# Performance work log

Hardware: AMD Instinct MI355X
Metric: run time of the kernel (lower is better)

## Reference

```python
import jax, jax.numpy as jnp
import numpy as np

B, T, R = 64, 256, 256          # batch, timepoints, n_rois (T==R required by bmm path)
H, NH, DH, FF, LAT, L = 256, 8, 32, 512, 64, 2
EPS = 1e-5


def layernorm(x, g, b):
    m = x.mean(-1, keepdims=True)
    v = ((x - m) ** 2).mean(-1, keepdims=True)
    return (x - m) / jnp.sqrt(v + EPS) * g + b


def leaky_relu(x):
    return jnp.where(x >= 0, x, 0.1 * x)


def setup_inputs() -> dict:
    key = jax.random.key(0)
    ks = iter(jax.random.split(key, 64))
    def nrm(shape, s=0.02):
        return jax.random.normal(next(ks), shape, jnp.float32) * s
    return {
        "x": jax.random.normal(next(ks), (B, T, R), jnp.float32),
        "node_view": jax.random.normal(next(ks), (B, R, R), jnp.float32) * 0.1,
        "edge_view": jax.random.normal(next(ks), (B, R, R), jnp.float32) * 0.1,
        "fp_w": nrm((H, R)), "fp_b": jnp.zeros((H,)),
        "fp_g": jnp.ones((H,)), "fp_beta": jnp.zeros((H,)),
        "qkv_w": nrm((L, 3 * H, H)), "qkv_b": jnp.zeros((L, 3 * H)),
        "attn_out_w": nrm((L, H, H)), "attn_out_b": jnp.zeros((L, H)),
        "ln1_g": jnp.ones((L, H)), "ln1_b": jnp.zeros((L, H)),
        "ff1_w": nrm((L, FF, H)), "ff1_b": jnp.zeros((L, FF)),
        "ff2_w": nrm((L, H, FF)), "ff2_b": jnp.zeros((L, H)),
        "ln2_g": jnp.ones((L, H)), "ln2_b": jnp.zeros((L, H)),
        "out_w": nrm((R, H)), "out_b": jnp.zeros((R,)),
        "mu_w1": nrm((H // 2, H)), "mu_b1": jnp.zeros((H // 2,)),
        "mu_g": jnp.ones((H // 2,)), "mu_beta": jnp.zeros((H // 2,)),
        "mu_w2": nrm((LAT, H // 2)), "mu_b2": jnp.zeros((LAT,)),
        "lv_w1": nrm((H // 2, H)), "lv_b1": jnp.zeros((H // 2,)),
        "lv_g": jnp.ones((H // 2,)), "lv_beta": jnp.zeros((H // 2,)),
        "lv_w2": nrm((LAT, H // 2)), "lv_b2": jnp.zeros((LAT,)),
    }


def reference(x, node_view, edge_view, fp_w, fp_b, fp_g, fp_beta,
              qkv_w, qkv_b, attn_out_w, attn_out_b, ln1_g, ln1_b,
              ff1_w, ff1_b, ff2_w, ff2_b, ln2_g, ln2_b,
              out_w, out_b, mu_w1, mu_b1, mu_g, mu_beta, mu_w2, mu_b2,
              lv_w1, lv_b1, lv_g, lv_beta, lv_w2, lv_b2):
    # graph-view message passing: bmm(x^T, view), averaged, transposed back
    xr = jnp.swapaxes(x, 1, 2)                           # [B,R,T]
    msg = 0.5 * (jnp.einsum('brt,btq->brq', xr, node_view)
                 + jnp.einsum('brt,btq->brq', xr, edge_view))
    h = jnp.swapaxes(msg, 1, 2)                          # [B,T,R]
    # feature_proj: Linear -> LayerNorm -> LeakyReLU(0.1) -> Dropout(eval)
    h = leaky_relu(layernorm(h @ fp_w.T + fp_b, fp_g, fp_beta))  # [B,T,H]
    # TransformerEncoder (post-norm, relu FFN, dropout=identity)
    scale = 1.0 / jnp.sqrt(jnp.float32(DH))
    for i in range(L):
        qkv = h @ qkv_w[i].T + qkv_b[i]                  # [B,T,3H]
        q, k, v = jnp.split(qkv, 3, axis=-1)
        q = q.reshape(B, T, NH, DH).transpose(0, 2, 1, 3)
        k = k.reshape(B, T, NH, DH).transpose(0, 2, 1, 3)
        v = v.reshape(B, T, NH, DH).transpose(0, 2, 1, 3)
        attn = jax.nn.softmax(jnp.einsum('bhqd,bhkd->bhqk', q, k) * scale, axis=-1)
        o = jnp.einsum('bhqk,bhkd->bhqd', attn, v).transpose(0, 2, 1, 3).reshape(B, T, H)
        o = o @ attn_out_w[i].T + attn_out_b[i]
        h = layernorm(h + o, ln1_g[i], ln1_b[i])
        f = jax.nn.relu(h @ ff1_w[i].T + ff1_b[i]) @ ff2_w[i].T + ff2_b[i]
        h = layernorm(h + f, ln2_g[i], ln2_b[i])
    # fresh linear (treated as fixed params) then batched Pearson correlation
    y = h @ out_w.T + out_b                              # [B,T,R]
    data = jnp.swapaxes(y, 1, 2)                         # [B,R,T]
    c = data - data.mean(-1, keepdims=True)
    std = jnp.sqrt((c ** 2).sum(-1, keepdims=True) / (T - 1))   # unbiased, like torch.std
    cn = c / (std + 1e-8)
    corr = jnp.einsum('brt,bst->brs', cn, cn) / (T - 1)
    corr = jnp.nan_to_num(jnp.clip(corr, -1.0, 1.0), nan=0.0)   # [B,R,R]
    # heads
    pooled = h.mean(axis=1)                              # [B,H]
    mu = leaky_relu(layernorm(pooled @ mu_w1.T + mu_b1, mu_g, mu_beta)) @ mu_w2.T + mu_b2
    logvar = leaky_relu(layernorm(pooled @ lv_w1.T + lv_b1, lv_g, lv_beta)) @ lv_w2.T + lv_b2
    return mu, logvar, corr
```

## Files before the change

kernel.cpp:

```cpp
#include <hip/hip_runtime.h>
#include <hip/hip_bf16.h>
#include <math.h>

#define BB 64
#define NLAYER 2

typedef __attribute__((ext_vector_type(8))) short bfrag;
typedef __attribute__((ext_vector_type(4))) float f4_t;

__device__ __forceinline__ float dot4(float4 a, float4 b, float acc) {
    acc = fmaf(a.x, b.x, acc);
    acc = fmaf(a.y, b.y, acc);
    acc = fmaf(a.z, b.z, acc);
    acc = fmaf(a.w, b.w, acc);
    return acc;
}

__device__ __forceinline__ ushort f2bf(float f) {
    uint32_t u = __float_as_uint(f);
    uint32_t r = (u + 0x7FFFu + ((u >> 16) & 1u)) >> 16;
    return (ushort)r;
}
__device__ __forceinline__ float bf2f(ushort u) {
    return __uint_as_float(((uint32_t)u) << 16);
}

__global__ __launch_bounds__(256) void k_cvt(
    const float* __restrict__ fp_w, const float* __restrict__ qkv_w,
    const float* __restrict__ aow, const float* __restrict__ f1w,
    const float* __restrict__ f2w, const float* __restrict__ outw,
    ushort* __restrict__ dst) {
    const int g = blockIdx.x;
    const size_t idx = (size_t)g * 2048 + threadIdx.x * 8;
    const float* src;
    size_t base;
    if (g < 32)       { src = fp_w;  base = 0; }
    else if (g < 224) { src = qkv_w; base = 65536; }
    else if (g < 288) { src = aow;   base = 458752; }
    else if (g < 416) { src = f1w;   base = 589824; }
    else if (g < 544) { src = f2w;   base = 851968; }
    else              { src = outw;  base = 1114112; }
    const float4* s4 = reinterpret_cast<const float4*>(src + (idx - base));
    float4 a = s4[0], b = s4[1];
    bfrag o;
    o[0] = (short)f2bf(a.x); o[1] = (short)f2bf(a.y);
    o[2] = (short)f2bf(a.z); o[3] = (short)f2bf(a.w);
    o[4] = (short)f2bf(b.x); o[5] = (short)f2bf(b.y);
    o[6] = (short)f2bf(b.z); o[7] = (short)f2bf(b.w);
    *reinterpret_cast<bfrag*>(dst + idx) = o;
}

template <int EPI, bool WF32, bool WBF>
__global__ __launch_bounds__(256) void k_mm(
    const ushort* __restrict__ A, const ushort* __restrict__ B,
    const float* __restrict__ bias, float* __restrict__ C,
    ushort* __restrict__ Cb, int K, int N,
    size_t aStr, size_t bStr, size_t cStr) {
    __shared__ __align__(16) ushort As[64 * 72];
    __shared__ __align__(16) ushort Bs[128 * 72];
    const int tid = threadIdx.x;
    const int m0 = blockIdx.x * 64, n0 = blockIdx.y * 128;
    const size_t z = blockIdx.z;
    const int w = tid >> 6, lane = tid & 63;
    const int wm = w >> 1, wn = w & 1;
    const int fr = lane & 15, fq = lane >> 4;

    const int arow = tid >> 2, akc = (tid & 3) * 16;
    const ushort* aS = A + z * aStr + (size_t)(m0 + arow) * K + akc;
    ushort* aD = &As[arow * 72 + akc];
    const int brow = tid >> 1, bkc = (tid & 1) * 32;
    const ushort* bS = B + z * bStr + (size_t)(n0 + brow) * K + bkc;
    ushort* bD = &Bs[brow * 72 + bkc];

    f4_t acc[2][4];
#pragma unroll
    for (int i = 0; i < 2; ++i)
#pragma unroll
        for (int j = 0; j < 4; ++j) acc[i][j] = (f4_t)0.f;

    bfrag ra0, ra1, rb0, rb1, rb2, rb3;
    {
        const bfrag* ap = reinterpret_cast<const bfrag*>(aS);
        ra0 = ap[0]; ra1 = ap[1];
        const bfrag* bp = reinterpret_cast<const bfrag*>(bS);
        rb0 = bp[0]; rb1 = bp[1]; rb2 = bp[2]; rb3 = bp[3];
    }

    for (int k0 = 0; k0 < K; k0 += 64) {
        reinterpret_cast<bfrag*>(aD)[0] = ra0;
        reinterpret_cast<bfrag*>(aD)[1] = ra1;
        reinterpret_cast<bfrag*>(bD)[0] = rb0;
        reinterpret_cast<bfrag*>(bD)[1] = rb1;
        reinterpret_cast<bfrag*>(bD)[2] = rb2;
        reinterpret_cast<bfrag*>(bD)[3] = rb3;
        __syncthreads();
        if (k0 + 64 < K) {
            const bfrag* ap = reinterpret_cast<const bfrag*>(aS + k0 + 64);
            ra0 = ap[0]; ra1 = ap[1];
            const bfrag* bp = reinterpret_cast<const bfrag*>(bS + k0 + 64);
            rb0 = bp[0]; rb1 = bp[1]; rb2 = bp[2]; rb3 = bp[3];
        }
#pragma unroll
        for (int ks = 0; ks < 2; ++ks) {
            const int kb = ks * 32 + fq * 8;
            bfrag af[2], bf[4];
#pragma unroll
            for (int fm = 0; fm < 2; ++fm)
                af[fm] = *reinterpret_cast<const bfrag*>(
                    &As[(wm * 32 + fm * 16 + fr) * 72 + kb]);
#pragma unroll
            for (int fn = 0; fn < 4; ++fn)
                bf[fn] = *reinterpret_cast<const bfrag*>(
                    &Bs[(wn * 64 + fn * 16 + fr) * 72 + kb]);
#pragma unroll
            for (int fm = 0; fm < 2; ++fm)
#pragma unroll
                for (int fn = 0; fn < 4; ++fn)
                    acc[fm][fn] = __builtin_amdgcn_mfma_f32_16x16x32_bf16(
                        bf[fn], af[fm], acc[fm][fn], 0, 0, 0);
        }
        __syncthreads();
    }

#pragma unroll
    for (int fn = 0; fn < 4; ++fn) {
        const int col0 = n0 + wn * 64 + fn * 16 + fq * 4;
        float4 bv = make_float4(0.f, 0.f, 0.f, 0.f);
        if (EPI != 3 && bias != nullptr)
            bv = *reinterpret_cast<const float4*>(&bias[col0]);
#pragma unroll
        for (int fm = 0; fm < 2; ++fm) {
            const int row = m0 + wm * 32 + fm * 16 + fr;
            float v0 = acc[fm][fn][0] + bv.x;
            float v1 = acc[fm][fn][1] + bv.y;
            float v2 = acc[fm][fn][2] + bv.z;
            float v3 = acc[fm][fn][3] + bv.w;
            if (EPI == 2) {
                v0 = fmaxf(v0, 0.f); v1 = fmaxf(v1, 0.f);
                v2 = fmaxf(v2, 0.f); v3 = fmaxf(v3, 0.f);
            }
            if (EPI == 3) {
                v0 = acc[fm][fn][0] * (1.f / 255.f);
                v1 = acc[fm][fn][1] * (1.f / 255.f);
                v2 = acc[fm][fn][2] * (1.f / 255.f);
                v3 = acc[fm][fn][3] * (1.f / 255.f);
                if (v0 != v0) v0 = 0.f;
                if (v1 != v1) v1 = 0.f;
                if (v2 != v2) v2 = 0.f;
                if (v3 != v3) v3 = 0.f;
                v0 = fminf(1.f, fmaxf(-1.f, v0));
                v1 = fminf(1.f, fmaxf(-1.f, v1));
                v2 = fminf(1.f, fmaxf(-1.f, v2));
                v3 = fminf(1.f, fmaxf(-1.f, v3));
            }
            const size_t o = cStr * z + (size_t)row * N + col0;
            if (WF32) {
                float4 fv = {v0, v1, v2, v3};
                *reinterpret_cast<float4*>(&C[o]) = fv;
            }
            if (WBF) {
                ushort4 uv;
                uv.x = f2bf(v0); uv.y = f2bf(v1);
                uv.z = f2bf(v2); uv.w = f2bf(v3);
                *reinterpret_cast<ushort4*>(&Cb[o]) = uv;
            }
        }
    }
}

template <int ACT, bool RES>
__global__ __launch_bounds__(256) void k_mmln(
    const ushort* __restrict__ A, const ushort* __restrict__ W,
    const float* __restrict__ bias, const ushort* __restrict__ res,
    const float* __restrict__ g, const float* __restrict__ bt,
    ushort* __restrict__ outb, int K) {
    __shared__ __align__(16) ushort As[32 * 72];
    __shared__ __align__(16) ushort Bs[256 * 72];
    __shared__ float redS[32][4];
    __shared__ float redQ[32][4];
    const int tid = threadIdx.x;
    const int m0 = blockIdx.x * 32;
    const int w = tid >> 6, lane = tid & 63;
    const int fr = lane & 15, fq = lane >> 4;

    const int arow = tid >> 3, akc = (tid & 7) * 8;
    const ushort* aS = A + (size_t)(m0 + arow) * K + akc;
    ushort* aD = &As[arow * 72 + akc];
    const int brow = tid >> 1, bkc = (tid & 1) * 32;
    const ushort* bS0 = W + (size_t)brow * K + bkc;
    const ushort* bS1 = W + (size_t)(brow + 128) * K + bkc;
    ushort* bD0 = &Bs[brow * 72 + bkc];
    ushort* bD1 = &Bs[(brow + 128) * 72 + bkc];

    f4_t acc[2][4];
#pragma unroll
    for (int i = 0; i < 2; ++i)
#pragma unroll
        for (int j = 0; j < 4; ++j) acc[i][j] = (f4_t)0.f;

    bfrag ra, rb0, rb1, rb2, rb3, rc0, rc1, rc2, rc3;
    {
        ra = *reinterpret_cast<const bfrag*>(aS);
        const bfrag* bp0 = reinterpret_cast<const bfrag*>(bS0);
        rb0 = bp0[0]; rb1 = bp0[1]; rb2 = bp0[2]; rb3 = bp0[3];
        const bfrag* bp1 = reinterpret_cast<const bfrag*>(bS1);
        rc0 = bp1[0]; rc1 = bp1[1]; rc2 = bp1[2]; rc3 = bp1[3];
    }

    for (int k0 = 0; k0 < K; k0 += 64) {
        *reinterpret_cast<bfrag*>(aD) = ra;
        reinterpret_cast<bfrag*>(bD0)[0] = rb0;
        reinterpret_cast<bfrag*>(bD0)[1] = rb1;
        reinterpret_cast<bfrag*>(bD0)[2] = rb2;
        reinterpret_cast<bfrag*>(bD0)[3] = rb3;
        reinterpret_cast<bfrag*>(bD1)[0] = rc0;
        reinterpret_cast<bfrag*>(bD1)[1] = rc1;
        reinterpret_cast<bfrag*>(bD1)[2] = rc2;
        reinterpret_cast<bfrag*>(bD1)[3] = rc3;
        __syncthreads();
        if (k0 + 64 < K) {
            ra = *reinterpret_cast<const bfrag*>(aS + k0 + 64);
            const bfrag* bp0 = reinterpret_cast<const bfrag*>(bS0 + k0 + 64);
            rb0 = bp0[0]; rb1 = bp0[1]; rb2 = bp0[2]; rb3 = bp0[3];
            const bfrag* bp1 = reinterpret_cast<const bfrag*>(bS1 + k0 + 64);
            rc0 = bp1[0]; rc1 = bp1[1]; rc2 = bp1[2]; rc3 = bp1[3];
        }
#pragma unroll
        for (int ks = 0; ks < 2; ++ks) {
            const int kb = ks * 32 + fq * 8;
            bfrag af[2], bf[4];
#pragma unroll
            for (int fm = 0; fm < 2; ++fm)
                af[fm] = *reinterpret_cast<const bfrag*>(
                    &As[(fm * 16 + fr) * 72 + kb]);
#pragma unroll
            for (int fn = 0; fn < 4; ++fn)
                bf[fn] = *reinterpret_cast<const bfrag*>(
                    &Bs[(w * 64 + fn * 16 + fr) * 72 + kb]);
#pragma unroll
            for (int fm = 0; fm < 2; ++fm)
#pragma unroll
                for (int fn = 0; fn < 4; ++fn)
                    acc[fm][fn] = __builtin_amdgcn_mfma_f32_16x16x32_bf16(
                        bf[fn], af[fm], acc[fm][fn], 0, 0, 0);
        }
        __syncthreads();
    }

#pragma unroll
    for (int fn = 0; fn < 4; ++fn) {
        const int col0 = w * 64 + fn * 16 + fq * 4;
        const float4 bv = *reinterpret_cast<const float4*>(&bias[col0]);
#pragma unroll
        for (int fm = 0; fm < 2; ++fm) {
            const int row = fm * 16 + fr;
            float r0 = 0.f, r1 = 0.f, r2 = 0.f, r3 = 0.f;
            if (RES) {
                ushort4 r4 = *reinterpret_cast<const ushort4*>(
                    &res[(size_t)(m0 + row) * 256 + col0]);
                r0 = bf2f(r4.x); r1 = bf2f(r4.y);
                r2 = bf2f(r4.z); r3 = bf2f(r4.w);
            }
            acc[fm][fn][0] += bv.x + r0;
            acc[fm][fn][1] += bv.y + r1;
            acc[fm][fn][2] += bv.z + r2;
            acc[fm][fn][3] += bv.w + r3;
        }
    }
#pragma unroll
    for (int fm = 0; fm < 2; ++fm) {
        float s = 0.f, q = 0.f;
#pragma unroll
        for (int fn = 0; fn < 4; ++fn)
#pragma unroll
            for (int j = 0; j < 4; ++j) {
                const float v = acc[fm][fn][j];
                s += v;
                q += v * v;
            }
        s += __shfl_xor(s, 16); q += __shfl_xor(q, 16);
        s += __shfl_xor(s, 32); q += __shfl_xor(q, 32);
        if (fq == 0) {
            redS[fm * 16 + fr][w] = s;
            redQ[fm * 16 + fr][w] = q;
        }
    }
    __syncthreads();
#pragma unroll
    for (int fm = 0; fm < 2; ++fm) {
        const int row = fm * 16 + fr;
        const float S = redS[row][0] + redS[row][1] + redS[row][2] + redS[row][3];
        const float Q = redQ[row][0] + redQ[row][1] + redQ[row][2] + redQ[row][3];
        const float mean = S * (1.f / 256.f);
        const float var = Q * (1.f / 256.f) - mean * mean;
        const float rstd = rsqrtf(fmaxf(var, 0.f) + 1e-5f);
        const size_t rowoff = (size_t)(m0 + row) * 256;
#pragma unroll
        for (int fn = 0; fn < 4; ++fn) {
            const int col0 = w * 64 + fn * 16 + fq * 4;
            const float4 g4 = *reinterpret_cast<const float4*>(&g[col0]);
            const float4 b4 = *reinterpret_cast<const float4*>(&bt[col0]);
            float v0 = (acc[fm][fn][0] - mean) * rstd * g4.x + b4.x;
            float v1 = (acc[fm][fn][1] - mean) * rstd * g4.y + b4.y;
            float v2 = (acc[fm][fn][2] - mean) * rstd * g4.z + b4.z;
            float v3 = (acc[fm][fn][3] - mean) * rstd * g4.w + b4.w;
            if (ACT == 1) {
                v0 = v0 >= 0.f ? v0 : 0.1f * v0;
                v1 = v1 >= 0.f ? v1 : 0.1f * v1;
                v2 = v2 >= 0.f ? v2 : 0.1f * v2;
                v3 = v3 >= 0.f ? v3 : 0.1f * v3;
            }
            ushort4 uv;
            uv.x = f2bf(v0); uv.y = f2bf(v1);
            uv.z = f2bf(v2); uv.w = f2bf(v3);
            *reinterpret_cast<ushort4*>(&outb[rowoff + col0]) = uv;
        }
    }
}

__global__ __launch_bounds__(256) void k_attn2(const ushort* __restrict__ qkv,
                                               ushort* __restrict__ o) {
    const int h = blockIdx.x, b = blockIdx.y;
    const int tid = threadIdx.x;
    const int w = tid >> 6, lane = tid & 63;
    const int fr = lane & 15, fq = lane >> 4;

    __shared__ __align__(16) ushort Ks[256][40];
    __shared__ __align__(16) ushort Vt[32][264];
    __shared__ __align__(16) ushort Ps[4][64][40];

    const ushort* base = qkv + (size_t)b * 196608 + h * 32;

    {
        const bfrag* kp = reinterpret_cast<const bfrag*>(base + (size_t)tid * 768 + 256);
        bfrag k0 = kp[0], k1 = kp[1], k2 = kp[2], k3 = kp[3];
        *reinterpret_cast<bfrag*>(&Ks[tid][0]) = k0;
        *reinterpret_cast<bfrag*>(&Ks[tid][8]) = k1;
        *reinterpret_cast<bfrag*>(&Ks[tid][16]) = k2;
        *reinterpret_cast<bfrag*>(&Ks[tid][24]) = k3;
    }
    {
        const bfrag* vp = reinterpret_cast<const bfrag*>(base + (size_t)tid * 768 + 512);
        bfrag v0 = vp[0], v1 = vp[1], v2 = vp[2], v3 = vp[3];
#pragma unroll
        for (int e = 0; e < 8; ++e) {
            Vt[e][tid] = (ushort)v0[e];
            Vt[8 + e][tid] = (ushort)v1[e];
            Vt[16 + e][tid] = (ushort)v2[e];
            Vt[24 + e][tid] = (ushort)v3[e];
        }
    }
    const int q0 = w * 64;
    bfrag qf[4];
#pragma unroll
    for (int fm = 0; fm < 4; ++fm)
        qf[fm] = *reinterpret_cast<const bfrag*>(
            base + (size_t)(q0 + fm * 16 + fr) * 768 + fq * 8);
    __syncthreads();

    f4_t oacc[4][2];
    float rs[4][4];
#pragma unroll
    for (int fm = 0; fm < 4; ++fm) {
        oacc[fm][0] = (f4_t)0.f;
        oacc[fm][1] = (f4_t)0.f;
#pragma unroll
        for (int j = 0; j < 4; ++j) rs[fm][j] = 0.f;
    }
    const f4_t zero4 = (f4_t)0.f;
    const float qsl = 0.17677669529663687f * 1.4426950408889634f;

    for (int kt = 0; kt < 8; ++kt) {
        bfrag kf0 = *reinterpret_cast<const bfrag*>(&Ks[kt * 32 + fr][fq * 8]);
        bfrag kf1 = *reinterpret_cast<const bfrag*>(&Ks[kt * 32 + 16 + fr][fq * 8]);
        f4_t s0[4], s1[4];
#pragma unroll
        for (int fm = 0; fm < 4; ++fm) {
            s0[fm] = __builtin_amdgcn_mfma_f32_16x16x32_bf16(qf[fm], kf0, zero4, 0, 0, 0);
            s1[fm] = __builtin_amdgcn_mfma_f32_16x16x32_bf16(qf[fm], kf1, zero4, 0, 0, 0);
        }
#pragma unroll
        for (int fm = 0; fm < 4; ++fm) {
#pragma unroll
            for (int j = 0; j < 4; ++j) {
                const int row = fm * 16 + fq * 4 + j;
                ushort u0 = f2bf(exp2f(s0[fm][j] * qsl));
                ushort u1 = f2bf(exp2f(s1[fm][j] * qsl));
                Ps[w][row][fr] = u0;
                Ps[w][row][16 + fr] = u1;
                rs[fm][j] += bf2f(u0) + bf2f(u1);
            }
        }
        bfrag vf0 = *reinterpret_cast<const bfrag*>(&Vt[fr][kt * 32 + fq * 8]);
        bfrag vf1 = *reinterpret_cast<const bfrag*>(&Vt[16 + fr][kt * 32 + fq * 8]);
        bfrag pf[4];
#pragma unroll
        for (int fm = 0; fm < 4; ++fm)
            pf[fm] = *reinterpret_cast<const bfrag*>(&Ps[w][fm * 16 + fr][fq * 8]);
#pragma unroll
        for (int fm = 0; fm < 4; ++fm) {
            oacc[fm][0] = __builtin_amdgcn_mfma_f32_16x16x32_bf16(pf[fm], vf0, oacc[fm][0], 0, 0, 0);
            oacc[fm][1] = __builtin_amdgcn_mfma_f32_16x16x32_bf16(pf[fm], vf1, oacc[fm][1], 0, 0, 0);
        }
    }

#pragma unroll
    for (int fm = 0; fm < 4; ++fm)
#pragma unroll
        for (int j = 0; j < 4; ++j) {
            float r = rs[fm][j];
            r += __shfl_xor(r, 1);
            r += __shfl_xor(r, 2);
            r += __shfl_xor(r, 4);
            r += __shfl_xor(r, 8);
            rs[fm][j] = 1.f / r;
        }
    ushort* ob = o + (size_t)b * 65536 + h * 32;
#pragma unroll
    for (int fm = 0; fm < 4; ++fm) {
        const int qrow = q0 + fm * 16 + fq * 4;
#pragma unroll
        for (int j = 0; j < 4; ++j) {
            const float inv = rs[fm][j];
            ob[(size_t)(qrow + j) * 256 + fr] = f2bf(oacc[fm][0][j] * inv);
            ob[(size_t)(qrow + j) * 256 + 16 + fr] = f2bf(oacc[fm][1][j] * inv);
        }
    }
}

__global__ __launch_bounds__(256) void k_xpose_bmm(
    const float* __restrict__ x, const float* __restrict__ nv,
    const float* __restrict__ ev, ushort* __restrict__ At,
    ushort* __restrict__ Xt) {
    const int b = blockIdx.z;
    const int k0 = blockIdx.x * 64, i0 = blockIdx.y * 64;
    __shared__ float TA[64][65];
    __shared__ float TX[64][65];
    const size_t bb = (size_t)b * 65536;
    const int tid = threadIdx.x;
    const int lr = tid >> 4, lc = (tid & 15) * 4;
#pragma unroll
    for (int l = 0; l < 4; ++l) {
        const int row = lr + l * 16;
        const size_t gidx = bb + (size_t)(k0 + row) * 256 + i0 + lc;
        float4 n4 = *reinterpret_cast<const float4*>(nv + gidx);
        float4 e4 = *reinterpret_cast<const float4*>(ev + gidx);
        float4 x4 = *reinterpret_cast<const float4*>(x + gidx);
        TA[row][lc] = 0.5f * (n4.x + e4.x);
        TA[row][lc + 1] = 0.5f * (n4.y + e4.y);
        TA[row][lc + 2] = 0.5f * (n4.z + e4.z);
        TA[row][lc + 3] = 0.5f * (n4.w + e4.w);
        TX[row][lc] = x4.x;
        TX[row][lc + 1] = x4.y;
        TX[row][lc + 2] = x4.z;
        TX[row][lc + 3] = x4.w;
    }
    __syncthreads();
    const int i = tid & 63, kk = (tid >> 6) * 16;
    bfrag a0, a1, x0, x1;
#pragma unroll
    for (int e = 0; e < 8; ++e) {
        a0[e] = (short)f2bf(TA[kk + e][i]);
        a1[e] = (short)f2bf(TA[kk + 8 + e][i]);
        x0[e] = (short)f2bf(TX[kk + e][i]);
        x1[e] = (short)f2bf(TX[kk + 8 + e][i]);
    }
    const size_t o = bb + (size_t)(i0 + i) * 256 + k0 + kk;
    *reinterpret_cast<bfrag*>(At + o) = a0;
    *reinterpret_cast<bfrag*>(At + o + 8) = a1;
    *reinterpret_cast<bfrag*>(Xt + o) = x0;
    *reinterpret_cast<bfrag*>(Xt + o + 8) = x1;
}

__global__ __launch_bounds__(256) void k_pstats(const ushort* __restrict__ y,
                                                ushort* __restrict__ cnT) {
    const int b = blockIdx.y, r0 = blockIdx.x * 64;
    __shared__ __align__(16) ushort T[256][72];
    __shared__ float sred[4][64];
    __shared__ float qred[4][64];
    __shared__ float mstat[64];
    __shared__ float istat[64];
    const int tid = threadIdx.x;
    {
        const bfrag* yv = reinterpret_cast<const bfrag*>(
            y + (size_t)b * 65536 + (size_t)tid * 256 + r0);
#pragma unroll
        for (int i = 0; i < 8; ++i)
            *reinterpret_cast<bfrag*>(&T[tid][i * 8]) = yv[i];
    }
    __syncthreads();
    const int rl = tid & 63, tc = tid >> 6;
    {
        float s = 0.f, q = 0.f;
        for (int t = 0; t < 64; ++t) {
            float v = bf2f(T[tc * 64 + t][rl]);
            s += v;
            q += v * v;
        }
        sred[tc][rl] = s;
        qred[tc][rl] = q;
    }
    __syncthreads();
    if (tid < 64) {
        const float S = sred[0][tid] + sred[1][tid] + sred[2][tid] + sred[3][tid];
        const float Q = qred[0][tid] + qred[1][tid] + qred[2][tid] + qred[3][tid];
        const float mean = S * (1.f / 256.f);
        const float var = (Q - S * mean) * (1.f / 255.f);
        const float stdv = sqrtf(fmaxf(var, 0.f));
        mstat[tid] = mean;
        istat[tid] = 1.f / (stdv + 1e-8f);
    }
    __syncthreads();
    const float mean = mstat[rl], inv = istat[rl];
    ushort* dst = cnT + (size_t)b * 65536 + (size_t)(r0 + rl) * 256 + tc * 64;
#pragma unroll
    for (int i = 0; i < 8; ++i) {
        bfrag c;
#pragma unroll
        for (int e = 0; e < 8; ++e)
            c[e] = (short)f2bf((bf2f(T[tc * 64 + i * 8 + e][rl]) - mean) * inv);
        reinterpret_cast<bfrag*>(dst)[i] = c;
    }
}

__global__ __launch_bounds__(1024) void k_pool(const ushort* __restrict__ h,
                                               float* __restrict__ pooled) {
    const int b = blockIdx.x;
    const int c = threadIdx.x & 255, tc = threadIdx.x >> 8;
    const ushort* hb = h + (size_t)b * 65536 + (size_t)tc * 64 * 256;
    float s = 0.f;
    for (int t = 0; t < 64; ++t) s += bf2f(hb[t * 256 + c]);
    __shared__ float pp[4][256];
    pp[tc][c] = s;
    __syncthreads();
    if (tc == 0)
        pooled[b * 256 + c] = (pp[0][c] + pp[1][c] + pp[2][c] + pp[3][c]) * (1.f / 256.f);
}

__global__ __launch_bounds__(128) void k_head(
    const float* __restrict__ pooled,
    const float* __restrict__ mw1, const float* __restrict__ mb1,
    const float* __restrict__ mg, const float* __restrict__ mbt,
    const float* __restrict__ mw2, const float* __restrict__ mb2,
    const float* __restrict__ lw1, const float* __restrict__ lb1,
    const float* __restrict__ lg, const float* __restrict__ lbt,
    const float* __restrict__ lw2, const float* __restrict__ lb2,
    float* __restrict__ outp) {
    const int b = blockIdx.x, hd = blockIdx.y;
    const int tid = threadIdx.x;
    const float* w1 = hd ? lw1 : mw1;
    const float* b1 = hd ? lb1 : mb1;
    const float* g = hd ? lg : mg;
    const float* bt = hd ? lbt : mbt;
    const float* w2 = hd ? lw2 : mw2;
    const float* b2 = hd ? lb2 : mb2;

    __shared__ float pl[256];
    __shared__ float t1[128];
    __shared__ float redS[2];
    __shared__ float redQ[2];

    pl[tid] = pooled[b * 256 + tid];
    pl[tid + 128] = pooled[b * 256 + tid + 128];
    __syncthreads();

    float a = b1[tid];
    const float4* w1v = (const float4*)(w1 + (size_t)tid * 256);
#pragma unroll 4
    for (int k4 = 0; k4 < 64; ++k4) {
        float4 w = w1v[k4];
        float4 p = *(const float4*)&pl[k4 * 4];
        a = dot4(p, w, a);
    }
    float s = a, q = a * a;
#pragma unroll
    for (int m = 1; m < 64; m <<= 1) {
        s += __shfl_xor(s, m);
        q += __shfl_xor(q, m);
    }
    if ((tid & 63) == 0) { redS[tid >> 6] = s; redQ[tid >> 6] = q; }
    __syncthreads();
    const float mean = (redS[0] + redS[1]) * (1.f / 128.f);
    const float var = (redQ[0] + redQ[1]) * (1.f / 128.f) - mean * mean;
    const float rstd = rsqrtf(fmaxf(var, 0.f) + 1e-5f);
    float v = (a - mean) * rstd * g[tid] + bt[tid];
    v = v >= 0.f ? v : 0.1f * v;
    t1[tid] = v;
    __syncthreads();
    if (tid < 64) {
        float o = b2[tid];
        const float* w2r = w2 + (size_t)tid * 128;
#pragma unroll 4
        for (int c = 0; c < 128; ++c) o = fmaf(t1[c], w2r[c], o);
        outp[hd * 4096 + b * 64 + tid] = o;
    }
}

extern "C" void kernel_launch(void* const* d_in, const int* in_sizes, int n_in,
                              void* d_out, int out_size, void* d_ws, size_t ws_size,
                              hipStream_t stream) {
    const float* x = (const float*)d_in[0];
    const float* nv = (const float*)d_in[1];
    const float* ev = (const float*)d_in[2];
    const float* fp_w = (const float*)d_in[3];
    const float* fp_b = (const float*)d_in[4];
    const float* fp_g = (const float*)d_in[5];
    const float* fp_beta = (const float*)d_in[6];
    const float* qkv_w = (const float*)d_in[7];
    const float* qkv_b = (const float*)d_in[8];
    const float* aow = (const float*)d_in[9];
    const float* aob = (const float*)d_in[10];
    const float* ln1g = (const float*)d_in[11];
    const float* ln1b = (const float*)d_in[12];
    const float* f1w = (const float*)d_in[13];
    const float* f1b = (const float*)d_in[14];
    const float* f2w = (const float*)d_in[15];
    const float* f2b = (const float*)d_in[16];
    const float* ln2g = (const float*)d_in[17];
    const float* ln2b = (const float*)d_in[18];
    const float* outw = (const float*)d_in[19];
    const float* outb = (const float*)d_in[20];
    const float* muw1 = (const float*)d_in[21];
    const float* mub1 = (const float*)d_in[22];
    const float* mug = (const float*)d_in[23];
    const float* mubt = (const float*)d_in[24];
    const float* muw2 = (const float*)d_in[25];
    const float* mub2 = (const float*)d_in[26];
    const float* lvw1 = (const float*)d_in[27];
    const float* lvb1 = (const float*)d_in[28];
    const float* lvg = (const float*)d_in[29];
    const float* lvbt = (const float*)d_in[30];
    const float* lvw2 = (const float*)d_in[31];
    const float* lvb2 = (const float*)d_in[32];

    float* out = (float*)d_out;
    float* ws = (float*)d_ws;

    float* pooled = ws;
    ushort* ub = (ushort*)(ws + 32768);
    ushort* wh_bf = ub;
    ushort* qkvb = ub + 4194304;
    ushort* At = qkvb;
    ushort* Xt = qkvb + 4194304;
    ushort* o_bf = ub + 16777216;
    ushort* h0_bf = o_bf;
    ushort* f1_bf = ub + 20971520;
    ushort* cnT = f1_bf;
    ushort* y_bf = ub + 29360128;
    ushort* wbf = ub + 33554432;

    k_cvt<<<576, 256, 0, stream>>>(fp_w, qkv_w, aow, f1w, f2w, outw, wbf);

    k_xpose_bmm<<<dim3(4, 4, BB), 256, 0, stream>>>(x, nv, ev, At, Xt);
    k_mm<0, false, true><<<dim3(4, 2, BB), 256, 0, stream>>>(
        At, Xt, nullptr, nullptr, h0_bf, 256, 256, 65536, 65536, 65536);

    k_mmln<1, false><<<512, 256, 0, stream>>>(
        h0_bf, wbf, fp_b, nullptr, fp_g, fp_beta, wh_bf, 256);

    for (int l = 0; l < NLAYER; ++l) {
        k_mm<0, false, true><<<dim3(256, 6, 1), 256, 0, stream>>>(
            wh_bf, wbf + 65536 + (size_t)l * 196608, qkv_b + l * 768,
            nullptr, qkvb, 256, 768, 0, 0, 0);
        k_attn2<<<dim3(8, BB), 256, 0, stream>>>(qkvb, o_bf);
        k_mmln<0, true><<<512, 256, 0, stream>>>(
            o_bf, wbf + 458752 + (size_t)l * 65536, aob + l * 256,
            wh_bf, ln1g + l * 256, ln1b + l * 256, wh_bf, 256);
        k_mm<2, false, true><<<dim3(256, 4, 1), 256, 0, stream>>>(
            wh_bf, wbf + 589824 + (size_t)l * 131072, f1b + l * 512,
            nullptr, f1_bf, 256, 512, 0, 0, 0);
        k_mmln<0, true><<<512, 256, 0, stream>>>(
            f1_bf, wbf + 851968 + (size_t)l * 131072, f2b + l * 256,
            wh_bf, ln2g + l * 256, ln2b + l * 256, wh_bf, 512);
    }

    k_mm<0, false, true><<<dim3(256, 2, 1), 256, 0, stream>>>(
        wh_bf, wbf + 1114112, outb, nullptr, y_bf, 256, 256, 0, 0, 0);

    k_pstats<<<dim3(4, BB), 256, 0, stream>>>(y_bf, cnT);
    k_mm<3, true, false><<<dim3(4, 2, BB), 256, 0, stream>>>(
        cnT, cnT, nullptr, out + 8192, nullptr, 256, 256, 65536, 65536, 65536);

    k_pool<<<BB, 1024, 0, stream>>>(wh_bf, pooled);
    k_head<<<dim3(BB, 2), 128, 0, stream>>>(
        pooled, muw1, mub1, mug, mubt, muw2, mub2,
        lvw1, lvb1, lvg, lvbt, lvw2, lvb2, out);
}
```

Before: 252.3 us.

## Fuse QKV projection into attention kernel and merge pool with heads

The per-layer QKV GEMM is folded into the attention kernel. Each (head, batch) block computes its own 256x96 Q/K/V slice from the hidden state directly into shared memory, so the 768-wide qkv intermediate is never written to or read back from global memory, and one launch per layer is removed. The pooling and mu/logvar head kernels are also merged into a single launch. In exchange the fused kernel uses about 108KB of shared memory, which limits occupancy to roughly one block per CU, and its GEMM runs without double buffering, so there is less parallelism per launch.

Measured after the change: 261.3 us. +3.5%, slower.

```diff
diff --git a/kernel.cpp b/kernel.cpp
--- a/kernel.cpp
+++ b/kernel.cpp
@@ -318,45 +318,117 @@
     }
 }
 
-__global__ __launch_bounds__(256) void k_attn2(const ushort* __restrict__ qkv,
-                                               ushort* __restrict__ o) {
-    const int h = blockIdx.x, b = blockIdx.y;
+__global__ __launch_bounds__(256) void k_qkvattn(
+    const ushort* __restrict__ hbuf, const ushort* __restrict__ Wqkv,
+    const float* __restrict__ bias, ushort* __restrict__ o) {
+    __shared__ __align__(16) ushort smem[54272];
+    ushort* As = smem;
+    ushort* Ws = smem + 18432;
+    ushort (*Ps)[64][40] = (ushort(*)[64][40])smem;
+    ushort (*Qs)[40] = (ushort(*)[40])(smem + 25344);
+    ushort (*Ks)[40] = (ushort(*)[40])(smem + 35584);
+    ushort (*Vt)[264] = (ushort(*)[264])(smem + 45824);
+
+    const int hd = blockIdx.x, b = blockIdx.y;
     const int tid = threadIdx.x;
     const int w = tid >> 6, lane = tid & 63;
     const int fr = lane & 15, fq = lane >> 4;
 
-    __shared__ __align__(16) ushort Ks[256][40];
-    __shared__ __align__(16) ushort Vt[32][264];
-    __shared__ __align__(16) ushort Ps[4][64][40];
-
-    const ushort* base = qkv + (size_t)b * 196608 + h * 32;
-
-    {
-        const bfrag* kp = reinterpret_cast<const bfrag*>(base + (size_t)tid * 768 + 256);
-        bfrag k0 = kp[0], k1 = kp[1], k2 = kp[2], k3 = kp[3];
-        *reinterpret_cast<bfrag*>(&Ks[tid][0]) = k0;
-        *reinterpret_cast<bfrag*>(&Ks[tid][8]) = k1;
-        *reinterpret_cast<bfrag*>(&Ks[tid][16]) = k2;
-        *reinterpret_cast<bfrag*>(&Ks[tid][24]) = k3;
-    }
-    {
-        const bfrag* vp = reinterpret_cast<const bfrag*>(base + (size_t)tid * 768 + 512);
-        bfrag v0 = vp[0], v1 = vp[1], v2 = vp[2], v3 = vp[3];
-#pragma unroll
-        for (int e = 0; e < 8; ++e) {
-            Vt[e][tid] = (ushort)v0[e];
-            Vt[8 + e][tid] = (ushort)v1[e];
-            Vt[16 + e][tid] = (ushort)v2[e];
-            Vt[24 + e][tid] = (ushort)v3[e];
-        }
-    }
+    const ushort* aS = hbuf + (size_t)b * 65536 + (size_t)tid * 256;
+    int wgrow = 0;
+    if (tid < 192) {
+        const int r96 = tid >> 1;
+        wgrow = r96 < 32 ? hd * 32 + r96
+              : (r96 < 64 ? 256 + hd * 32 + (r96 - 32)
+                          : 512 + hd * 32 + (r96 - 64));
+    }
+
+    f4_t acc[4][6];
+#pragma unroll
+    for (int i = 0; i < 4; ++i)
+#pragma unroll
+        for (int j = 0; j < 6; ++j) acc[i][j] = (f4_t)0.f;
+
+    for (int k0 = 0; k0 < 256; k0 += 64) {
+        {
+            const bfrag* ap = reinterpret_cast<const bfrag*>(aS + k0);
+            bfrag a0 = ap[0], a1 = ap[1], a2 = ap[2], a3 = ap[3];
+            bfrag a4 = ap[4], a5 = ap[5], a6 = ap[6], a7 = ap[7];
+            bfrag* ad = reinterpret_cast<bfrag*>(&As[tid * 72]);
+            ad[0] = a0; ad[1] = a1; ad[2] = a2; ad[3] = a3;
+            ad[4] = a4; ad[5] = a5; ad[6] = a6; ad[7] = a7;
+            if (tid < 192) {
+                const int r96 = tid >> 1, hf = (tid & 1) * 32;
+                const bfrag* wp = reinterpret_cast<const bfrag*>(
+                    Wqkv + (size_t)wgrow * 256 + k0 + hf);
+                bfrag w0 = wp[0], w1 = wp[1], w2 = wp[2], w3 = wp[3];
+                bfrag* wd = reinterpret_cast<bfrag*>(&Ws[r96 * 72 + hf]);
+                wd[0] = w0; wd[1] = w1; wd[2] = w2; wd[3] = w3;
+            }
+        }
+        __syncthreads();
+#pragma unroll
+        for (int ks = 0; ks < 2; ++ks) {
+            const int kb = ks * 32 + fq * 8;
+            bfrag af[4], bf[6];
+#pragma unroll
+            for (int fm = 0; fm < 4; ++fm)
+                af[fm] = *reinterpret_cast<const bfrag*>(
+                    &As[(w * 64 + fm * 16 + fr) * 72 + kb]);
+#pragma unroll
+            for (int cf = 0; cf < 6; ++cf)
+                bf[cf] = *reinterpret_cast<const bfrag*>(
+                    &Ws[(cf * 16 + fr) * 72 + kb]);
+#pragma unroll
+            for (int fm = 0; fm < 4; ++fm)
+#pragma unroll
+                for (int cf = 0; cf < 6; ++cf)
+                    acc[fm][cf] = __builtin_amdgcn_mfma_f32_16x16x32_bf16(
+                        bf[cf], af[fm], acc[fm][cf], 0, 0, 0);
+        }
+        __syncthreads();
+    }
+
+#pragma unroll
+    for (int cf = 0; cf < 6; ++cf) {
+        const int c0 = cf * 16 + fq * 4;
+        const int cl = c0 & 31;
+        const int gbase = (cf < 2) ? hd * 32 + cl
+                        : (cf < 4) ? 256 + hd * 32 + cl
+                                   : 512 + hd * 32 + cl;
+        const float4 bv = *reinterpret_cast<const float4*>(&bias[gbase]);
+#pragma unroll
+        for (int fm = 0; fm < 4; ++fm) {
+            const int row = w * 64 + fm * 16 + fr;
+            float v0 = acc[fm][cf][0] + bv.x;
+            float v1 = acc[fm][cf][1] + bv.y;
+            float v2 = acc[fm][cf][2] + bv.z;
+            float v3 = acc[fm][cf][3] + bv.w;
+            if (cf < 2) {
+                ushort4 uv;
+                uv.x = f2bf(v0); uv.y = f2bf(v1);
+                uv.z = f2bf(v2); uv.w = f2bf(v3);
+                *reinterpret_cast<ushort4*>(&Qs[row][cl]) = uv;
+            } else if (cf < 4) {
+                ushort4 uv;
+                uv.x = f2bf(v0); uv.y = f2bf(v1);
+                uv.z = f2bf(v2); uv.w = f2bf(v3);
+                *reinterpret_cast<ushort4*>(&Ks[row][cl]) = uv;
+            } else {
+                Vt[cl + 0][row] = f2bf(v0);
+                Vt[cl + 1][row] = f2bf(v1);
+                Vt[cl + 2][row] = f2bf(v2);
+                Vt[cl + 3][row] = f2bf(v3);
+            }
+        }
+    }
+    __syncthreads();
+
     const int q0 = w * 64;
     bfrag qf[4];
 #pragma unroll
     for (int fm = 0; fm < 4; ++fm)
-        qf[fm] = *reinterpret_cast<const bfrag*>(
-            base + (size_t)(q0 + fm * 16 + fr) * 768 + fq * 8);
-    __syncthreads();
+        qf[fm] = *reinterpret_cast<const bfrag*>(&Qs[q0 + fm * 16 + fr][fq * 8]);
 
     f4_t oacc[4][2];
     float rs[4][4];
@@ -415,7 +487,7 @@
             r += __shfl_xor(r, 8);
             rs[fm][j] = 1.f / r;
         }
-    ushort* ob = o + (size_t)b * 65536 + h * 32;
+    ushort* ob = o + (size_t)b * 65536 + hd * 32;
 #pragma unroll
     for (int fm = 0; fm < 4; ++fm) {
         const int qrow = q0 + fm * 16 + fq * 4;
@@ -523,22 +595,8 @@
     }
 }
 
-__global__ __launch_bounds__(1024) void k_pool(const ushort* __restrict__ h,
-                                               float* __restrict__ pooled) {
-    const int b = blockIdx.x;
-    const int c = threadIdx.x & 255, tc = threadIdx.x >> 8;
-    const ushort* hb = h + (size_t)b * 65536 + (size_t)tc * 64 * 256;
-    float s = 0.f;
-    for (int t = 0; t < 64; ++t) s += bf2f(hb[t * 256 + c]);
-    __shared__ float pp[4][256];
-    pp[tc][c] = s;
-    __syncthreads();
-    if (tc == 0)
-        pooled[b * 256 + c] = (pp[0][c] + pp[1][c] + pp[2][c] + pp[3][c]) * (1.f / 256.f);
-}
-
-__global__ __launch_bounds__(128) void k_head(
-    const float* __restrict__ pooled,
+__global__ __launch_bounds__(512) void k_poolhead(
+    const ushort* __restrict__ h,
     const float* __restrict__ mw1, const float* __restrict__ mb1,
     const float* __restrict__ mg, const float* __restrict__ mbt,
     const float* __restrict__ mw2, const float* __restrict__ mb2,
@@ -546,53 +604,68 @@
     const float* __restrict__ lg, const float* __restrict__ lbt,
     const float* __restrict__ lw2, const float* __restrict__ lb2,
     float* __restrict__ outp) {
-    const int b = blockIdx.x, hd = blockIdx.y;
-    const int tid = threadIdx.x;
-    const float* w1 = hd ? lw1 : mw1;
-    const float* b1 = hd ? lb1 : mb1;
-    const float* g = hd ? lg : mg;
-    const float* bt = hd ? lbt : mbt;
-    const float* w2 = hd ? lw2 : mw2;
-    const float* b2 = hd ? lb2 : mb2;
-
-    __shared__ float pl[256];
-    __shared__ float t1[128];
-    __shared__ float redS[2];
-    __shared__ float redQ[2];
-
-    pl[tid] = pooled[b * 256 + tid];
-    pl[tid + 128] = pooled[b * 256 + tid + 128];
-    __syncthreads();
-
-    float a = b1[tid];
-    const float4* w1v = (const float4*)(w1 + (size_t)tid * 256);
+    const int b = blockIdx.x, tid = threadIdx.x;
+    __shared__ float pp[2][256];
+    __shared__ float pooled[256];
+    __shared__ float rS[4], rQ[4];
+    __shared__ float t1[2][128];
+
+    {
+        const int c = tid & 255, tc = tid >> 8;
+        const ushort* hb = h + (size_t)b * 65536 + (size_t)tc * 128 * 256 + c;
+        float s = 0.f;
+        for (int t = 0; t < 128; ++t) s += bf2f(hb[(size_t)t * 256]);
+        pp[tc][c] = s;
+    }
+    __syncthreads();
+    if (tid < 256) pooled[tid] = (pp[0][tid] + pp[1][tid]) * (1.f / 256.f);
+    __syncthreads();
+
+    float a = 0.f;
+    if (tid < 256) {
+        const int hd = tid >> 7, u = tid & 127;
+        const float* w1 = hd ? lw1 : mw1;
+        const float* b1 = hd ? lb1 : mb1;
+        a = b1[u];
+        const float4* w1v = reinterpret_cast<const float4*>(w1 + (size_t)u * 256);
 #pragma unroll 4
-    for (int k4 = 0; k4 < 64; ++k4) {
-        float4 w = w1v[k4];
-        float4 p = *(const float4*)&pl[k4 * 4];
-        a = dot4(p, w, a);
-    }
-    float s = a, q = a * a;
-#pragma unroll
-    for (int m = 1; m < 64; m <<= 1) {
-        s += __shfl_xor(s, m);
-        q += __shfl_xor(q, m);
-    }
-    if ((tid & 63) == 0) { redS[tid >> 6] = s; redQ[tid >> 6] = q; }
-    __syncthreads();
-    const float mean = (redS[0] + redS[1]) * (1.f / 128.f);
-    const float var = (redQ[0] + redQ[1]) * (1.f / 128.f) - mean * mean;
-    const float rstd = rsqrtf(fmaxf(var, 0.f) + 1e-5f);
-    float v = (a - mean) * rstd * g[tid] + bt[tid];
-    v = v >= 0.f ? v : 0.1f * v;
-    t1[tid] = v;
-    __syncthreads();
-    if (tid < 64) {
-        float o = b2[tid];
-        const float* w2r = w2 + (size_t)tid * 128;
+        for (int k4 = 0; k4 < 64; ++k4) {
+            float4 wv = w1v[k4];
+            float4 p = *reinterpret_cast<const float4*>(&pooled[k4 * 4]);
+            a = dot4(p, wv, a);
+        }
+        float s = a, q = a * a;
+#pragma unroll
+        for (int m = 1; m < 64; m <<= 1) {
+            s += __shfl_xor(s, m);
+            q += __shfl_xor(q, m);
+        }
+        if ((tid & 63) == 0) { rS[tid >> 6] = s; rQ[tid >> 6] = q; }
+    }
+    __syncthreads();
+    if (tid < 256) {
+        const int hd = tid >> 7, u = tid & 127;
+        const float* g = hd ? lg : mg;
+        const float* bt = hd ? lbt : mbt;
+        const float S = rS[hd * 2] + rS[hd * 2 + 1];
+        const float Q = rQ[hd * 2] + rQ[hd * 2 + 1];
+        const float mean = S * (1.f / 128.f);
+        const float var = Q * (1.f / 128.f) - mean * mean;
+        const float rstd = rsqrtf(fmaxf(var, 0.f) + 1e-5f);
+        float v = (a - mean) * rstd * g[u] + bt[u];
+        v = v >= 0.f ? v : 0.1f * v;
+        t1[hd][u] = v;
+    }
+    __syncthreads();
+    if (tid < 128) {
+        const int hd = tid >> 6, ou = tid & 63;
+        const float* w2 = hd ? lw2 : mw2;
+        const float* b2 = hd ? lb2 : mb2;
+        float o = b2[ou];
+        const float* w2r = w2 + (size_t)ou * 128;
 #pragma unroll 4
-        for (int c = 0; c < 128; ++c) o = fmaf(t1[c], w2r[c], o);
-        outp[hd * 4096 + b * 64 + tid] = o;
+        for (int c = 0; c < 128; ++c) o = fmaf(t1[hd][c], w2r[c], o);
+        outp[hd * 4096 + b * 64 + ou] = o;
     }
 }
 
@@ -636,12 +709,10 @@
     float* out = (float*)d_out;
     float* ws = (float*)d_ws;
 
-    float* pooled = ws;
-    ushort* ub = (ushort*)(ws + 32768);
+    ushort* ub = (ushort*)ws;
     ushort* wh_bf = ub;
-    ushort* qkvb = ub + 4194304;
-    ushort* At = qkvb;
-    ushort* Xt = qkvb + 4194304;
+    ushort* At = ub + 4194304;
+    ushort* Xt = ub + 8388608;
     ushort* o_bf = ub + 16777216;
     ushort* h0_bf = o_bf;
     ushort* f1_bf = ub + 20971520;
@@ -659,10 +730,8 @@
         h0_bf, wbf, fp_b, nullptr, fp_g, fp_beta, wh_bf, 256);
 
     for (int l = 0; l < NLAYER; ++l) {
-        k_mm<0, false, true><<<dim3(256, 6, 1), 256, 0, stream>>>(
-            wh_bf, wbf + 65536 + (size_t)l * 196608, qkv_b + l * 768,
-            nullptr, qkvb, 256, 768, 0, 0, 0);
-        k_attn2<<<dim3(8, BB), 256, 0, stream>>>(qkvb, o_bf);
+        k_qkvattn<<<dim3(8, BB), 256, 0, stream>>>(
+            wh_bf, wbf + 65536 + (size_t)l * 196608, qkv_b + l * 768, o_bf);
         k_mmln<0, true><<<512, 256, 0, stream>>>(
             o_bf, wbf + 458752 + (size_t)l * 65536, aob + l * 256,
             wh_bf, ln1g + l * 256, ln1b + l * 256, wh_bf, 256);
@@ -681,8 +750,7 @@
     k_mm<3, true, false><<<dim3(4, 2, BB), 256, 0, stream>>>(
         cnT, cnT, nullptr, out + 8192, nullptr, 256, 256, 65536, 65536, 65536);
 
-    k_pool<<<BB, 1024, 0, stream>>>(wh_bf, pooled);
-    k_head<<<dim3(BB, 2), 128, 0, stream>>>(
-        pooled, muw1, mub1, mug, mubt, muw2, mub2,
+    k_poolhead<<<BB, 512, 0, stream>>>(
+        wh_bf, muw1, mub1, mug, mubt, muw2, mub2,
         lvw1, lvb1, lvg, lvbt, lvw2, lvb2, out);
 }
```
